# Kernel optimization log

Hardware: AMD Instinct MI355X
Metric: run time of the kernel (lower is better)

The kernel has to match this reference:

```python
import jax, jax.numpy as jnp
import numpy as np

FP8_MAX = 448.0  # max normal of float8_e4m3fn (TE fwd format)
EPS = 1e-12


def _fp8_quant_dequant(t):
    """Per-tensor amax scaling -> cast to e4m3 -> dequant back to f32.
    Mirrors TE's per-tensor scaling recipe (scale = FP8_MAX / amax)."""
    amax = jnp.max(jnp.abs(t))
    scale = FP8_MAX / jnp.maximum(amax, EPS)
    q = jnp.clip(t * scale, -FP8_MAX, FP8_MAX).astype(jnp.float8_e4m3fn)
    return q.astype(jnp.float32) / scale


def setup_inputs() -> dict:
    key = jax.random.key(0)
    k1, k2, k3 = jax.random.split(key, 3)
    tokens, d_in, d_out = 8192, 4096, 4096
    x = jax.random.normal(k1, (tokens, d_in), dtype=jnp.float32)
    # kaiming_uniform_(a=sqrt(5)) -> U(-bound, bound), bound = sqrt(6/((1+a^2)*fan_in)) = 1/sqrt(fan_in)
    bound = 1.0 / np.sqrt(d_in)
    weight = jax.random.uniform(k2, (d_out, d_in), dtype=jnp.float32, minval=-bound, maxval=bound)
    bias = jnp.zeros((d_out,), dtype=jnp.float32) + 0.01 * jax.random.normal(k3, (d_out,), dtype=jnp.float32)
    return {"x": x, "weight": weight, "bias": bias}


def reference(x, weight, bias):
    # fp8 quant/dequant of activations and weights, then GEMM + bias
    xq = _fp8_quant_dequant(x)            # [T, Din]
    wq = _fp8_quant_dequant(weight)       # [Dout, Din]
    out = jnp.einsum("ti,oi->to", xq, wq) # [T, Dout]
    return out + bias[None, :]
```

## Files before the change

kernel.cpp:

```cpp
#include <hip/hip_runtime.h>
#include <stdint.h>

#define M_DIM 8192
#define N_DIM 4096
#define K_DIM 4096

typedef float f32x4 __attribute__((ext_vector_type(4)));
typedef int   i32x4 __attribute__((ext_vector_type(4)));
typedef int   i32x8 __attribute__((ext_vector_type(8)));

__global__ __launch_bounds__(256) void amax2_kernel(const float* __restrict__ x,
                                                    const float* __restrict__ wgt,
                                                    unsigned int* __restrict__ ws_u) {
    const int which = blockIdx.y;
    const float4* p = (const float4*)(which ? wgt : x);
    const int n4 = (which ? N_DIM : M_DIM) * (K_DIM / 4);
    int tid = blockIdx.x * blockDim.x + threadIdx.x;
    int stride = gridDim.x * blockDim.x;
    float m = 0.0f;
    for (int i = tid; i < n4; i += stride) {
        float4 v = p[i];
        m = fmaxf(m, fmaxf(fmaxf(fabsf(v.x), fabsf(v.y)),
                           fmaxf(fabsf(v.z), fabsf(v.w))));
    }
#pragma unroll
    for (int off = 32; off > 0; off >>= 1)
        m = fmaxf(m, __shfl_down(m, off, 64));
    __shared__ float sm[4];
    if ((threadIdx.x & 63) == 0) sm[threadIdx.x >> 6] = m;
    __syncthreads();
    if (threadIdx.x == 0) {
        m = fmaxf(fmaxf(sm[0], sm[1]), fmaxf(sm[2], sm[3]));
        atomicMax(ws_u + which, __float_as_uint(m));
    }
}

__global__ __launch_bounds__(256) void quant2_kernel(const float* __restrict__ x,
                                                     const float* __restrict__ wgt,
                                                     unsigned int* __restrict__ xq,
                                                     unsigned int* __restrict__ wq,
                                                     const unsigned int* __restrict__ ws_u) {
    const int which = blockIdx.y;
    const float4* p = (const float4*)(which ? wgt : x);
    unsigned int* outp = which ? wq : xq;
    const int n4 = (which ? N_DIM : M_DIM) * (K_DIM / 4);
    float amax = fmaxf(__uint_as_float(ws_u[which]), 1e-12f);
    float scale = 448.0f / amax;
    int tid = blockIdx.x * blockDim.x + threadIdx.x;
    int stride = gridDim.x * blockDim.x;
    for (int i = tid; i < n4; i += stride) {
        float4 v = p[i];
        float a = fminf(fmaxf(v.x * scale, -448.0f), 448.0f);
        float b = fminf(fmaxf(v.y * scale, -448.0f), 448.0f);
        float c = fminf(fmaxf(v.z * scale, -448.0f), 448.0f);
        float d = fminf(fmaxf(v.w * scale, -448.0f), 448.0f);
        int w = __builtin_amdgcn_cvt_pk_fp8_f32(a, b, 0, false);
        w = __builtin_amdgcn_cvt_pk_fp8_f32(c, d, w, true);
        outp[i] = (unsigned int)w;
    }
}

__device__ __forceinline__ void gld16(const void* g, void* l) {
    __builtin_amdgcn_global_load_lds(
        (const __attribute__((address_space(1))) void*)g,
        (__attribute__((address_space(3))) void*)l, 16, 0, 0);
}

#define MFMA_MX(a, b, c) __builtin_amdgcn_mfma_scale_f32_16x16x128_f8f6f4( \
    (a), (b), (c), 0, 0, 0, 0x7F7F7F7F, 0, 0x7F7F7F7F)

__global__ __launch_bounds__(512, 2) void gemm_fp8_kernel(
    const uint8_t* __restrict__ Aq,
    const uint8_t* __restrict__ Bq,
    const float* __restrict__ bias,
    const unsigned int* __restrict__ ws_u,
    float* __restrict__ out)
{
    __shared__ uint8_t lds[131072];

    const int tid = threadIdx.x;
    const int w = tid >> 6, l = tid & 63;

    const int cpx = (int)gridDim.x >> 3;
    const int bid = (int)blockIdx.x;
    const int swz = (bid & 7) * cpx + (bid >> 3);
    const int bm = swz >> 4, bn = swz & 15;

    const uint8_t* gA = Aq + (size_t)bm * 256 * K_DIM;
    const uint8_t* gB = Bq + (size_t)bn * 256 * K_DIM;

    const int idx = tid >> 3, p = tid & 7;
    const int srcX = ((p ^ (idx & 7)) << 4);
    const uint8_t* aRow = gA + (size_t)idx * K_DIM + srcX;
    const uint8_t* bRow = gB + (size_t)idx * K_DIM + srcX;

    const int wr = w >> 2, wc = w & 3;
    const int lr = l & 15, g = l >> 4;
    const int oLo = (((2 * g) ^ (lr & 7)) << 4);
    const int oHi = (((2 * g + 1) ^ (lr & 7)) << 4);
    const int rowA0 = wr * 128 + lr;
    const int rowB0 = wc * 64 + lr;

    auto stageAll = [&](int bb, int t1) {
        const size_t k0 = (size_t)t1 * 128;
        uint8_t* la = &lds[bb * 32768 + tid * 16];
        uint8_t* lb = &lds[65536 + bb * 32768 + tid * 16];
#pragma unroll
        for (int r = 0; r < 4; ++r)
            gld16(aRow + (size_t)(r << 6) * K_DIM + k0, la + r * 8192);
#pragma unroll
        for (int r = 0; r < 4; ++r)
            gld16(bRow + (size_t)(r << 6) * K_DIM + k0, lb + r * 8192);
    };
    auto ldf = [&](const uint8_t* base, int row) -> i32x8 {
        const uint8_t* q = base + (row << 7);
        i32x4 lo = *(const i32x4*)(q + oLo);
        i32x4 hi = *(const i32x4*)(q + oHi);
        return __builtin_shufflevector(lo, hi, 0, 1, 2, 3, 4, 5, 6, 7);
    };

    f32x4 acc[8][4] = {};

    stageAll(0, 0);

#pragma unroll 2
    for (int t = 0; t < 32; ++t) {
        const int buf = t & 1;
        const uint8_t* lab = &lds[buf * 32768];
        const uint8_t* lbb = &lds[65536 + buf * 32768];

        __builtin_amdgcn_s_barrier();
        if (t < 31) {
            stageAll(buf ^ 1, t + 1);
            asm volatile("s_waitcnt vmcnt(8)" ::: "memory");
        } else {
            asm volatile("s_waitcnt vmcnt(0)" ::: "memory");
        }
        __builtin_amdgcn_s_barrier();

        i32x8 bv0 = ldf(lbb, rowB0);
        i32x8 bv1 = ldf(lbb, rowB0 + 16);
        i32x8 av0 = ldf(lab, rowA0);
        i32x8 av1 = ldf(lab, rowA0 + 16);
        i32x8 av2 = ldf(lab, rowA0 + 32);
        i32x8 av3 = ldf(lab, rowA0 + 48);
        i32x8 bv2 = ldf(lbb, rowB0 + 32);
        i32x8 bv3 = ldf(lbb, rowB0 + 48);
        i32x8 av4 = ldf(lab, rowA0 + 64);
        i32x8 av5 = ldf(lab, rowA0 + 80);
        i32x8 av6 = ldf(lab, rowA0 + 96);
        i32x8 av7 = ldf(lab, rowA0 + 112);

        __builtin_amdgcn_s_setprio(1);
        acc[0][0] = MFMA_MX(av0, bv0, acc[0][0]);
        acc[0][1] = MFMA_MX(av0, bv1, acc[0][1]);
        acc[1][0] = MFMA_MX(av1, bv0, acc[1][0]);
        acc[1][1] = MFMA_MX(av1, bv1, acc[1][1]);
        acc[2][0] = MFMA_MX(av2, bv0, acc[2][0]);
        acc[2][1] = MFMA_MX(av2, bv1, acc[2][1]);
        acc[3][0] = MFMA_MX(av3, bv0, acc[3][0]);
        acc[3][1] = MFMA_MX(av3, bv1, acc[3][1]);
        acc[0][2] = MFMA_MX(av0, bv2, acc[0][2]);
        acc[0][3] = MFMA_MX(av0, bv3, acc[0][3]);
        acc[1][2] = MFMA_MX(av1, bv2, acc[1][2]);
        acc[1][3] = MFMA_MX(av1, bv3, acc[1][3]);
        acc[2][2] = MFMA_MX(av2, bv2, acc[2][2]);
        acc[2][3] = MFMA_MX(av2, bv3, acc[2][3]);
        acc[3][2] = MFMA_MX(av3, bv2, acc[3][2]);
        acc[3][3] = MFMA_MX(av3, bv3, acc[3][3]);
        acc[4][0] = MFMA_MX(av4, bv0, acc[4][0]);
        acc[4][1] = MFMA_MX(av4, bv1, acc[4][1]);
        acc[5][0] = MFMA_MX(av5, bv0, acc[5][0]);
        acc[5][1] = MFMA_MX(av5, bv1, acc[5][1]);
        acc[6][0] = MFMA_MX(av6, bv0, acc[6][0]);
        acc[6][1] = MFMA_MX(av6, bv1, acc[6][1]);
        acc[7][0] = MFMA_MX(av7, bv0, acc[7][0]);
        acc[7][1] = MFMA_MX(av7, bv1, acc[7][1]);
        acc[4][2] = MFMA_MX(av4, bv2, acc[4][2]);
        acc[4][3] = MFMA_MX(av4, bv3, acc[4][3]);
        acc[5][2] = MFMA_MX(av5, bv2, acc[5][2]);
        acc[5][3] = MFMA_MX(av5, bv3, acc[5][3]);
        acc[6][2] = MFMA_MX(av6, bv2, acc[6][2]);
        acc[6][3] = MFMA_MX(av6, bv3, acc[6][3]);
        acc[7][2] = MFMA_MX(av7, bv2, acc[7][2]);
        acc[7][3] = MFMA_MX(av7, bv3, acc[7][3]);
        __builtin_amdgcn_s_setprio(0);
    }

    const float ax = fmaxf(__uint_as_float(ws_u[0]), 1e-12f);
    const float aw = fmaxf(__uint_as_float(ws_u[1]), 1e-12f);
    const float inv = (ax * (1.0f / 448.0f)) * (aw * (1.0f / 448.0f));

    const int orow0 = bm * 256 + wr * 128 + g * 4;
    const int ocol0 = bn * 256 + wc * 64 + lr;
#pragma unroll
    for (int mb = 0; mb < 8; ++mb) {
#pragma unroll
        for (int nb = 0; nb < 4; ++nb) {
            const int col = ocol0 + nb * 16;
            const float bvv = bias[col];
#pragma unroll
            for (int j = 0; j < 4; ++j) {
                const int row = orow0 + mb * 16 + j;
                out[(size_t)row * N_DIM + col] = acc[mb][nb][j] * inv + bvv;
            }
        }
    }
}

extern "C" void kernel_launch(void* const* d_in, const int* in_sizes, int n_in,
                              void* d_out, int out_size, void* d_ws, size_t ws_size,
                              hipStream_t stream) {
    const float* x    = (const float*)d_in[0];
    const float* wgt  = (const float*)d_in[1];
    const float* bias = (const float*)d_in[2];
    float* out = (float*)d_out;

    unsigned int* ws_u = (unsigned int*)d_ws;
    uint8_t* xq = (uint8_t*)d_ws + 256;
    uint8_t* wq = xq + (size_t)M_DIM * K_DIM;

    hipMemsetAsync(d_ws, 0, 8, stream);

    dim3 ga(1024, 2);
    amax2_kernel<<<ga, 256, 0, stream>>>(x, wgt, ws_u);

    dim3 gq(2048, 2);
    quant2_kernel<<<gq, 256, 0, stream>>>(x, wgt, (unsigned int*)xq,
                                          (unsigned int*)wq, ws_u);

    gemm_fp8_kernel<<<(M_DIM / 256) * (N_DIM / 256), 512, 0, stream>>>(
        xq, wq, bias, ws_u, out);
}
```

Measured before the change: 236.4 us.

## Load B operand directly into registers, stage only A through LDS

```diff
diff --git a/kernel.cpp b/kernel.cpp
--- a/kernel.cpp
+++ b/kernel.cpp
@@ -68,6 +68,66 @@
 
 #define MFMA_MX(a, b, c) __builtin_amdgcn_mfma_scale_f32_16x16x128_f8f6f4( \
     (a), (b), (c), 0, 0, 0, 0x7F7F7F7F, 0, 0x7F7F7F7F)
+#define BAR()    __builtin_amdgcn_s_barrier()
+#define VMCNT(n) asm volatile("s_waitcnt vmcnt(" #n ")" ::: "memory")
+#define PRIO1()  __builtin_amdgcn_s_setprio(1)
+#define PRIO0()  __builtin_amdgcn_s_setprio(0)
+
+#define TILE_BODY(T, BC, BN)                                                   \
+  {                                                                            \
+    const uint8_t* lab = &lds[((T) & 1) * 32768];                              \
+    const int nb = (((T) & 1) ^ 1);                                            \
+    const int kn = ((T) + 1) * 128;                                            \
+    stA(nb, kn, 0);   stA(nb, kn, 64);                                         \
+    stA(nb, kn, 128); stA(nb, kn, 192);                                        \
+    BN[0] = *(const i32x8*)(bP0 + kn);                                         \
+    BN[1] = *(const i32x8*)(bP1 + kn);                                         \
+    BN[2] = *(const i32x8*)(bP2 + kn);                                         \
+    BN[3] = *(const i32x8*)(bP3 + kn);                                         \
+    av[0] = ldf(lab, rowA0);      av[1] = ldf(lab, rowA0 + 16);                \
+    av[2] = ldf(lab, rowA0 + 32); av[3] = ldf(lab, rowA0 + 48);                \
+    VMCNT(12);                                                                 \
+    PRIO1();                                                                   \
+    acc[0][0] = MFMA_MX(av[0], BC[0], acc[0][0]);                              \
+    acc[0][1] = MFMA_MX(av[0], BC[1], acc[0][1]);                              \
+    acc[1][0] = MFMA_MX(av[1], BC[0], acc[1][0]);                              \
+    acc[1][1] = MFMA_MX(av[1], BC[1], acc[1][1]);                              \
+    acc[2][0] = MFMA_MX(av[2], BC[0], acc[2][0]);                              \
+    acc[2][1] = MFMA_MX(av[2], BC[1], acc[2][1]);                              \
+    acc[3][0] = MFMA_MX(av[3], BC[0], acc[3][0]);                              \
+    acc[3][1] = MFMA_MX(av[3], BC[1], acc[3][1]);                              \
+    acc[0][2] = MFMA_MX(av[0], BC[2], acc[0][2]);                              \
+    acc[0][3] = MFMA_MX(av[0], BC[3], acc[0][3]);                              \
+    acc[1][2] = MFMA_MX(av[1], BC[2], acc[1][2]);                              \
+    acc[1][3] = MFMA_MX(av[1], BC[3], acc[1][3]);                              \
+    acc[2][2] = MFMA_MX(av[2], BC[2], acc[2][2]);                              \
+    acc[2][3] = MFMA_MX(av[2], BC[3], acc[2][3]);                              \
+    acc[3][2] = MFMA_MX(av[3], BC[2], acc[3][2]);                              \
+    acc[3][3] = MFMA_MX(av[3], BC[3], acc[3][3]);                              \
+    PRIO0();                                                                   \
+    av[0] = ldf(lab, rowA0 + 64); av[1] = ldf(lab, rowA0 + 80);                \
+    av[2] = ldf(lab, rowA0 + 96); av[3] = ldf(lab, rowA0 + 112);               \
+    PRIO1();                                                                   \
+    acc[4][0] = MFMA_MX(av[0], BC[0], acc[4][0]);                              \
+    acc[4][1] = MFMA_MX(av[0], BC[1], acc[4][1]);                              \
+    acc[5][0] = MFMA_MX(av[1], BC[0], acc[5][0]);                              \
+    acc[5][1] = MFMA_MX(av[1], BC[1], acc[5][1]);                              \
+    acc[6][0] = MFMA_MX(av[2], BC[0], acc[6][0]);                              \
+    acc[6][1] = MFMA_MX(av[2], BC[1], acc[6][1]);                              \
+    acc[7][0] = MFMA_MX(av[3], BC[0], acc[7][0]);                              \
+    acc[7][1] = MFMA_MX(av[3], BC[1], acc[7][1]);                              \
+    acc[4][2] = MFMA_MX(av[0], BC[2], acc[4][2]);                              \
+    acc[4][3] = MFMA_MX(av[0], BC[3], acc[4][3]);                              \
+    acc[5][2] = MFMA_MX(av[1], BC[2], acc[5][2]);                              \
+    acc[5][3] = MFMA_MX(av[1], BC[3], acc[5][3]);                              \
+    acc[6][2] = MFMA_MX(av[2], BC[2], acc[6][2]);                              \
+    acc[6][3] = MFMA_MX(av[2], BC[3], acc[6][3]);                              \
+    acc[7][2] = MFMA_MX(av[3], BC[2], acc[7][2]);                              \
+    acc[7][3] = MFMA_MX(av[3], BC[3], acc[7][3]);                              \
+    PRIO0();                                                                   \
+    VMCNT(8);                                                                  \
+    BAR();                                                                     \
+  }
 
 __global__ __launch_bounds__(512, 2) void gemm_fp8_kernel(
     const uint8_t* __restrict__ Aq,
@@ -76,7 +136,7 @@
     const unsigned int* __restrict__ ws_u,
     float* __restrict__ out)
 {
-    __shared__ uint8_t lds[131072];
+    __shared__ uint8_t lds[65536];
 
     const int tid = threadIdx.x;
     const int w = tid >> 6, l = tid & 63;
@@ -87,30 +147,27 @@
     const int bm = swz >> 4, bn = swz & 15;
 
     const uint8_t* gA = Aq + (size_t)bm * 256 * K_DIM;
-    const uint8_t* gB = Bq + (size_t)bn * 256 * K_DIM;
 
     const int idx = tid >> 3, p = tid & 7;
     const int srcX = ((p ^ (idx & 7)) << 4);
     const uint8_t* aRow = gA + (size_t)idx * K_DIM + srcX;
-    const uint8_t* bRow = gB + (size_t)idx * K_DIM + srcX;
+    const int dA = tid * 16;
 
     const int wr = w >> 2, wc = w & 3;
     const int lr = l & 15, g = l >> 4;
     const int oLo = (((2 * g) ^ (lr & 7)) << 4);
     const int oHi = (((2 * g + 1) ^ (lr & 7)) << 4);
     const int rowA0 = wr * 128 + lr;
-    const int rowB0 = wc * 64 + lr;
-
-    auto stageAll = [&](int bb, int t1) {
-        const size_t k0 = (size_t)t1 * 128;
-        uint8_t* la = &lds[bb * 32768 + tid * 16];
-        uint8_t* lb = &lds[65536 + bb * 32768 + tid * 16];
-#pragma unroll
-        for (int r = 0; r < 4; ++r)
-            gld16(aRow + (size_t)(r << 6) * K_DIM + k0, la + r * 8192);
-#pragma unroll
-        for (int r = 0; r < 4; ++r)
-            gld16(bRow + (size_t)(r << 6) * K_DIM + k0, lb + r * 8192);
+
+    const uint8_t* bBase = Bq + (size_t)(bn * 256 + wc * 64 + lr) * K_DIM + g * 32;
+    const uint8_t* bP0 = bBase;
+    const uint8_t* bP1 = bBase + (size_t)16 * K_DIM;
+    const uint8_t* bP2 = bBase + (size_t)32 * K_DIM;
+    const uint8_t* bP3 = bBase + (size_t)48 * K_DIM;
+
+    auto stA = [&](int bb, int kn, int rbase) {
+        gld16(aRow + (size_t)rbase * K_DIM + kn,
+              &lds[bb * 32768 + rbase * 128 + dA]);
     };
     auto ldf = [&](const uint8_t* base, int row) -> i32x8 {
         const uint8_t* q = base + (row << 7);
@@ -120,71 +177,44 @@
     };
 
     f32x4 acc[8][4] = {};
-
-    stageAll(0, 0);
-
-#pragma unroll 2
-    for (int t = 0; t < 32; ++t) {
-        const int buf = t & 1;
-        const uint8_t* lab = &lds[buf * 32768];
-        const uint8_t* lbb = &lds[65536 + buf * 32768];
-
-        __builtin_amdgcn_s_barrier();
-        if (t < 31) {
-            stageAll(buf ^ 1, t + 1);
-            asm volatile("s_waitcnt vmcnt(8)" ::: "memory");
-        } else {
-            asm volatile("s_waitcnt vmcnt(0)" ::: "memory");
+    i32x8 av[4];
+    i32x8 b0[4], b1[4];
+
+    stA(0, 0, 0);   stA(0, 0, 64);
+    stA(0, 0, 128); stA(0, 0, 192);
+    b0[0] = *(const i32x8*)(bP0);
+    b0[1] = *(const i32x8*)(bP1);
+    b0[2] = *(const i32x8*)(bP2);
+    b0[3] = *(const i32x8*)(bP3);
+    VMCNT(8); BAR();
+
+    for (int t = 0; t < 30; t += 2) {
+        TILE_BODY(t, b0, b1);
+        TILE_BODY(t + 1, b1, b0);
+    }
+    TILE_BODY(30, b0, b1);
+
+    {
+        const uint8_t* lab = &lds[32768];
+        av[0] = ldf(lab, rowA0);      av[1] = ldf(lab, rowA0 + 16);
+        av[2] = ldf(lab, rowA0 + 32); av[3] = ldf(lab, rowA0 + 48);
+        VMCNT(0);
+#pragma unroll
+        for (int m = 0; m < 4; ++m) {
+            acc[m][0] = MFMA_MX(av[m], b1[0], acc[m][0]);
+            acc[m][1] = MFMA_MX(av[m], b1[1], acc[m][1]);
+            acc[m][2] = MFMA_MX(av[m], b1[2], acc[m][2]);
+            acc[m][3] = MFMA_MX(av[m], b1[3], acc[m][3]);
         }
-        __builtin_amdgcn_s_barrier();
-
-        i32x8 bv0 = ldf(lbb, rowB0);
-        i32x8 bv1 = ldf(lbb, rowB0 + 16);
-        i32x8 av0 = ldf(lab, rowA0);
-        i32x8 av1 = ldf(lab, rowA0 + 16);
-        i32x8 av2 = ldf(lab, rowA0 + 32);
-        i32x8 av3 = ldf(lab, rowA0 + 48);
-        i32x8 bv2 = ldf(lbb, rowB0 + 32);
-        i32x8 bv3 = ldf(lbb, rowB0 + 48);
-        i32x8 av4 = ldf(lab, rowA0 + 64);
-        i32x8 av5 = ldf(lab, rowA0 + 80);
-        i32x8 av6 = ldf(lab, rowA0 + 96);
-        i32x8 av7 = ldf(lab, rowA0 + 112);
-
-        __builtin_amdgcn_s_setprio(1);
-        acc[0][0] = MFMA_MX(av0, bv0, acc[0][0]);
-        acc[0][1] = MFMA_MX(av0, bv1, acc[0][1]);
-        acc[1][0] = MFMA_MX(av1, bv0, acc[1][0]);
-        acc[1][1] = MFMA_MX(av1, bv1, acc[1][1]);
-        acc[2][0] = MFMA_MX(av2, bv0, acc[2][0]);
-        acc[2][1] = MFMA_MX(av2, bv1, acc[2][1]);
-        acc[3][0] = MFMA_MX(av3, bv0, acc[3][0]);
-        acc[3][1] = MFMA_MX(av3, bv1, acc[3][1]);
-        acc[0][2] = MFMA_MX(av0, bv2, acc[0][2]);
-        acc[0][3] = MFMA_MX(av0, bv3, acc[0][3]);
-        acc[1][2] = MFMA_MX(av1, bv2, acc[1][2]);
-        acc[1][3] = MFMA_MX(av1, bv3, acc[1][3]);
-        acc[2][2] = MFMA_MX(av2, bv2, acc[2][2]);
-        acc[2][3] = MFMA_MX(av2, bv3, acc[2][3]);
-        acc[3][2] = MFMA_MX(av3, bv2, acc[3][2]);
-        acc[3][3] = MFMA_MX(av3, bv3, acc[3][3]);
-        acc[4][0] = MFMA_MX(av4, bv0, acc[4][0]);
-        acc[4][1] = MFMA_MX(av4, bv1, acc[4][1]);
-        acc[5][0] = MFMA_MX(av5, bv0, acc[5][0]);
-        acc[5][1] = MFMA_MX(av5, bv1, acc[5][1]);
-        acc[6][0] = MFMA_MX(av6, bv0, acc[6][0]);
-        acc[6][1] = MFMA_MX(av6, bv1, acc[6][1]);
-        acc[7][0] = MFMA_MX(av7, bv0, acc[7][0]);
-        acc[7][1] = MFMA_MX(av7, bv1, acc[7][1]);
-        acc[4][2] = MFMA_MX(av4, bv2, acc[4][2]);
-        acc[4][3] = MFMA_MX(av4, bv3, acc[4][3]);
-        acc[5][2] = MFMA_MX(av5, bv2, acc[5][2]);
-        acc[5][3] = MFMA_MX(av5, bv3, acc[5][3]);
-        acc[6][2] = MFMA_MX(av6, bv2, acc[6][2]);
-        acc[6][3] = MFMA_MX(av6, bv3, acc[6][3]);
-        acc[7][2] = MFMA_MX(av7, bv2, acc[7][2]);
-        acc[7][3] = MFMA_MX(av7, bv3, acc[7][3]);
-        __builtin_amdgcn_s_setprio(0);
+        av[0] = ldf(lab, rowA0 + 64); av[1] = ldf(lab, rowA0 + 80);
+        av[2] = ldf(lab, rowA0 + 96); av[3] = ldf(lab, rowA0 + 112);
+#pragma unroll
+        for (int m = 0; m < 4; ++m) {
+            acc[4 + m][0] = MFMA_MX(av[m], b1[0], acc[4 + m][0]);
+            acc[4 + m][1] = MFMA_MX(av[m], b1[1], acc[4 + m][1]);
+            acc[4 + m][2] = MFMA_MX(av[m], b1[2], acc[4 + m][2]);
+            acc[4 + m][3] = MFMA_MX(av[m], b1[3], acc[4 + m][3]);
+        }
     }
 
     const float ax = fmaxf(__uint_as_float(ws_u[0]), 1e-12f);
@@ -196,13 +226,13 @@
 #pragma unroll
     for (int mb = 0; mb < 8; ++mb) {
 #pragma unroll
-        for (int nb = 0; nb < 4; ++nb) {
-            const int col = ocol0 + nb * 16;
+        for (int nb2 = 0; nb2 < 4; ++nb2) {
+            const int col = ocol0 + nb2 * 16;
             const float bvv = bias[col];
 #pragma unroll
             for (int j = 0; j < 4; ++j) {
                 const int row = orow0 + mb * 16 + j;
-                out[(size_t)row * N_DIM + col] = acc[mb][nb][j] * inv + bvv;
+                out[(size_t)row * N_DIM + col] = acc[mb][nb2][j] * inv + bvv;
             }
         }
     }
```

Measured after the change: 292.1 us. 1.24x slower.

## Shrink GEMM tile to 256x128 with single LDS buffer for higher occupancy

Applied to the files above, without the earlier changes.

```diff
diff --git a/kernel.cpp b/kernel.cpp
--- a/kernel.cpp
+++ b/kernel.cpp
@@ -68,15 +68,19 @@
 
 #define MFMA_MX(a, b, c) __builtin_amdgcn_mfma_scale_f32_16x16x128_f8f6f4( \
     (a), (b), (c), 0, 0, 0, 0x7F7F7F7F, 0, 0x7F7F7F7F)
-
-__global__ __launch_bounds__(512, 2) void gemm_fp8_kernel(
+#define BAR()    __builtin_amdgcn_s_barrier()
+#define VMCNT(n) asm volatile("s_waitcnt vmcnt(" #n ")" ::: "memory")
+#define PRIO1()  __builtin_amdgcn_s_setprio(1)
+#define PRIO0()  __builtin_amdgcn_s_setprio(0)
+
+__global__ __launch_bounds__(512, 4) void gemm_fp8_kernel(
     const uint8_t* __restrict__ Aq,
     const uint8_t* __restrict__ Bq,
     const float* __restrict__ bias,
     const unsigned int* __restrict__ ws_u,
     float* __restrict__ out)
 {
-    __shared__ uint8_t lds[131072];
+    __shared__ uint8_t lds[49152];
 
     const int tid = threadIdx.x;
     const int w = tid >> 6, l = tid & 63;
@@ -84,117 +88,92 @@
     const int cpx = (int)gridDim.x >> 3;
     const int bid = (int)blockIdx.x;
     const int swz = (bid & 7) * cpx + (bid >> 3);
-    const int bm = swz >> 4, bn = swz & 15;
+    const int bm = swz >> 5, bn = swz & 31;
 
     const uint8_t* gA = Aq + (size_t)bm * 256 * K_DIM;
-    const uint8_t* gB = Bq + (size_t)bn * 256 * K_DIM;
+    const uint8_t* gB = Bq + (size_t)bn * 128 * K_DIM;
 
     const int idx = tid >> 3, p = tid & 7;
     const int srcX = ((p ^ (idx & 7)) << 4);
     const uint8_t* aRow = gA + (size_t)idx * K_DIM + srcX;
     const uint8_t* bRow = gB + (size_t)idx * K_DIM + srcX;
-
-    const int wr = w >> 2, wc = w & 3;
+    const int dA = tid * 16;
+
+    const int wr = w >> 1, wc = w & 1;
     const int lr = l & 15, g = l >> 4;
     const int oLo = (((2 * g) ^ (lr & 7)) << 4);
     const int oHi = (((2 * g + 1) ^ (lr & 7)) << 4);
-    const int rowA0 = wr * 128 + lr;
+    const int rowA0 = wr * 64 + lr;
     const int rowB0 = wc * 64 + lr;
 
-    auto stageAll = [&](int bb, int t1) {
-        const size_t k0 = (size_t)t1 * 128;
-        uint8_t* la = &lds[bb * 32768 + tid * 16];
-        uint8_t* lb = &lds[65536 + bb * 32768 + tid * 16];
-#pragma unroll
-        for (int r = 0; r < 4; ++r)
-            gld16(aRow + (size_t)(r << 6) * K_DIM + k0, la + r * 8192);
-#pragma unroll
-        for (int r = 0; r < 4; ++r)
-            gld16(bRow + (size_t)(r << 6) * K_DIM + k0, lb + r * 8192);
+    auto stage = [&](int kn) {
+        gld16(aRow + kn,                          &lds[dA]);
+        gld16(aRow + (size_t)64  * K_DIM + kn,    &lds[8192 + dA]);
+        gld16(aRow + (size_t)128 * K_DIM + kn,    &lds[16384 + dA]);
+        gld16(aRow + (size_t)192 * K_DIM + kn,    &lds[24576 + dA]);
+        gld16(bRow + kn,                          &lds[32768 + dA]);
+        gld16(bRow + (size_t)64  * K_DIM + kn,    &lds[40960 + dA]);
     };
-    auto ldf = [&](const uint8_t* base, int row) -> i32x8 {
-        const uint8_t* q = base + (row << 7);
+    auto ldfA = [&](int row) -> i32x8 {
+        const uint8_t* q = &lds[row << 7];
         i32x4 lo = *(const i32x4*)(q + oLo);
         i32x4 hi = *(const i32x4*)(q + oHi);
         return __builtin_shufflevector(lo, hi, 0, 1, 2, 3, 4, 5, 6, 7);
     };
-
-    f32x4 acc[8][4] = {};
-
-    stageAll(0, 0);
-
-#pragma unroll 2
+    auto ldfB = [&](int row) -> i32x8 {
+        const uint8_t* q = &lds[32768 + (row << 7)];
+        i32x4 lo = *(const i32x4*)(q + oLo);
+        i32x4 hi = *(const i32x4*)(q + oHi);
+        return __builtin_shufflevector(lo, hi, 0, 1, 2, 3, 4, 5, 6, 7);
+    };
+
+    f32x4 acc[4][4] = {};
+    i32x8 av[4], bv[2];
+
+    stage(0);
+
     for (int t = 0; t < 32; ++t) {
-        const int buf = t & 1;
-        const uint8_t* lab = &lds[buf * 32768];
-        const uint8_t* lbb = &lds[65536 + buf * 32768];
-
-        __builtin_amdgcn_s_barrier();
-        if (t < 31) {
-            stageAll(buf ^ 1, t + 1);
-            asm volatile("s_waitcnt vmcnt(8)" ::: "memory");
-        } else {
-            asm volatile("s_waitcnt vmcnt(0)" ::: "memory");
-        }
-        __builtin_amdgcn_s_barrier();
-
-        i32x8 bv0 = ldf(lbb, rowB0);
-        i32x8 bv1 = ldf(lbb, rowB0 + 16);
-        i32x8 av0 = ldf(lab, rowA0);
-        i32x8 av1 = ldf(lab, rowA0 + 16);
-        i32x8 av2 = ldf(lab, rowA0 + 32);
-        i32x8 av3 = ldf(lab, rowA0 + 48);
-        i32x8 bv2 = ldf(lbb, rowB0 + 32);
-        i32x8 bv3 = ldf(lbb, rowB0 + 48);
-        i32x8 av4 = ldf(lab, rowA0 + 64);
-        i32x8 av5 = ldf(lab, rowA0 + 80);
-        i32x8 av6 = ldf(lab, rowA0 + 96);
-        i32x8 av7 = ldf(lab, rowA0 + 112);
-
-        __builtin_amdgcn_s_setprio(1);
-        acc[0][0] = MFMA_MX(av0, bv0, acc[0][0]);
-        acc[0][1] = MFMA_MX(av0, bv1, acc[0][1]);
-        acc[1][0] = MFMA_MX(av1, bv0, acc[1][0]);
-        acc[1][1] = MFMA_MX(av1, bv1, acc[1][1]);
-        acc[2][0] = MFMA_MX(av2, bv0, acc[2][0]);
-        acc[2][1] = MFMA_MX(av2, bv1, acc[2][1]);
-        acc[3][0] = MFMA_MX(av3, bv0, acc[3][0]);
-        acc[3][1] = MFMA_MX(av3, bv1, acc[3][1]);
-        acc[0][2] = MFMA_MX(av0, bv2, acc[0][2]);
-        acc[0][3] = MFMA_MX(av0, bv3, acc[0][3]);
-        acc[1][2] = MFMA_MX(av1, bv2, acc[1][2]);
-        acc[1][3] = MFMA_MX(av1, bv3, acc[1][3]);
-        acc[2][2] = MFMA_MX(av2, bv2, acc[2][2]);
-        acc[2][3] = MFMA_MX(av2, bv3, acc[2][3]);
-        acc[3][2] = MFMA_MX(av3, bv2, acc[3][2]);
-        acc[3][3] = MFMA_MX(av3, bv3, acc[3][3]);
-        acc[4][0] = MFMA_MX(av4, bv0, acc[4][0]);
-        acc[4][1] = MFMA_MX(av4, bv1, acc[4][1]);
-        acc[5][0] = MFMA_MX(av5, bv0, acc[5][0]);
-        acc[5][1] = MFMA_MX(av5, bv1, acc[5][1]);
-        acc[6][0] = MFMA_MX(av6, bv0, acc[6][0]);
-        acc[6][1] = MFMA_MX(av6, bv1, acc[6][1]);
-        acc[7][0] = MFMA_MX(av7, bv0, acc[7][0]);
-        acc[7][1] = MFMA_MX(av7, bv1, acc[7][1]);
-        acc[4][2] = MFMA_MX(av4, bv2, acc[4][2]);
-        acc[4][3] = MFMA_MX(av4, bv3, acc[4][3]);
-        acc[5][2] = MFMA_MX(av5, bv2, acc[5][2]);
-        acc[5][3] = MFMA_MX(av5, bv3, acc[5][3]);
-        acc[6][2] = MFMA_MX(av6, bv2, acc[6][2]);
-        acc[6][3] = MFMA_MX(av6, bv3, acc[6][3]);
-        acc[7][2] = MFMA_MX(av7, bv2, acc[7][2]);
-        acc[7][3] = MFMA_MX(av7, bv3, acc[7][3]);
-        __builtin_amdgcn_s_setprio(0);
+        VMCNT(0);
+        BAR();
+
+        bv[0] = ldfB(rowB0);      bv[1] = ldfB(rowB0 + 16);
+        av[0] = ldfA(rowA0);      av[1] = ldfA(rowA0 + 16);
+        av[2] = ldfA(rowA0 + 32); av[3] = ldfA(rowA0 + 48);
+        PRIO1();
+        acc[0][0] = MFMA_MX(av[0], bv[0], acc[0][0]);
+        acc[0][1] = MFMA_MX(av[0], bv[1], acc[0][1]);
+        acc[1][0] = MFMA_MX(av[1], bv[0], acc[1][0]);
+        acc[1][1] = MFMA_MX(av[1], bv[1], acc[1][1]);
+        acc[2][0] = MFMA_MX(av[2], bv[0], acc[2][0]);
+        acc[2][1] = MFMA_MX(av[2], bv[1], acc[2][1]);
+        acc[3][0] = MFMA_MX(av[3], bv[0], acc[3][0]);
+        acc[3][1] = MFMA_MX(av[3], bv[1], acc[3][1]);
+        PRIO0();
+
+        bv[0] = ldfB(rowB0 + 32); bv[1] = ldfB(rowB0 + 48);
+        PRIO1();
+        acc[0][2] = MFMA_MX(av[0], bv[0], acc[0][2]);
+        acc[0][3] = MFMA_MX(av[0], bv[1], acc[0][3]);
+        acc[1][2] = MFMA_MX(av[1], bv[0], acc[1][2]);
+        acc[1][3] = MFMA_MX(av[1], bv[1], acc[1][3]);
+        acc[2][2] = MFMA_MX(av[2], bv[0], acc[2][2]);
+        acc[2][3] = MFMA_MX(av[2], bv[1], acc[2][3]);
+        acc[3][2] = MFMA_MX(av[3], bv[0], acc[3][2]);
+        acc[3][3] = MFMA_MX(av[3], bv[1], acc[3][3]);
+        PRIO0();
+
+        BAR();
+        if (t < 31) stage((t + 1) * 128);
     }
 
     const float ax = fmaxf(__uint_as_float(ws_u[0]), 1e-12f);
     const float aw = fmaxf(__uint_as_float(ws_u[1]), 1e-12f);
     const float inv = (ax * (1.0f / 448.0f)) * (aw * (1.0f / 448.0f));
 
-    const int orow0 = bm * 256 + wr * 128 + g * 4;
-    const int ocol0 = bn * 256 + wc * 64 + lr;
-#pragma unroll
-    for (int mb = 0; mb < 8; ++mb) {
+    const int orow0 = bm * 256 + wr * 64 + g * 4;
+    const int ocol0 = bn * 128 + wc * 64 + lr;
+#pragma unroll
+    for (int mb = 0; mb < 4; ++mb) {
 #pragma unroll
         for (int nb = 0; nb < 4; ++nb) {
             const int col = ocol0 + nb * 16;
@@ -229,6 +208,6 @@
     quant2_kernel<<<gq, 256, 0, stream>>>(x, wgt, (unsigned int*)xq,
                                           (unsigned int*)wq, ws_u);
 
-    gemm_fp8_kernel<<<(M_DIM / 256) * (N_DIM / 256), 512, 0, stream>>>(
+    gemm_fp8_kernel<<<(M_DIM / 256) * (N_DIM / 128), 512, 0, stream>>>(
         xq, wq, bias, ws_u, out);
 }
```

After: 230.6 us. 2.4% less time.
